# Kernel tuning notes

Hardware: AMD Instinct MI355X
Metric: run time of the kernel (lower is better)

## Reference

```python
import jax, jax.numpy as jnp
import numpy as np

B, S, D = 8, 1024, 768
H, DH = 8, 96          # number_of_heads, head_outdim = D // H
DFF = 4 * D            # mlp hidden
EPS = 1e-5


def _p(key, shape, scale=0.02):
    return (jax.random.normal(key, shape, dtype=jnp.float32) * scale)


def setup_inputs() -> dict:
    key = jax.random.key(0)
    ks = jax.random.split(key, 16)
    return {
        "h": jax.random.normal(ks[0], (B, S, D), dtype=jnp.float32),
        "x": jax.random.normal(ks[1], (B, S, D), dtype=jnp.float32),
        # SLN 1: scalar gamma/beta + LayerNorm affine
        "g1": jnp.ones((), jnp.float32), "be1": jnp.zeros((), jnp.float32),
        "ln1_w": jnp.ones((D,), jnp.float32), "ln1_b": jnp.zeros((D,), jnp.float32),
        # SLN 2
        "g2": jnp.ones((), jnp.float32), "be2": jnp.zeros((), jnp.float32),
        "ln2_w": jnp.ones((D,), jnp.float32), "ln2_b": jnp.zeros((D,), jnp.float32),
        # MSA projections (stored as [in, out] for x @ W)
        "Wq": _p(ks[2], (D, H * DH)), "bq": jnp.zeros((H * DH,), jnp.float32),
        "Wk": _p(ks[3], (D, H * DH)), "bk": jnp.zeros((H * DH,), jnp.float32),
        "Wv": _p(ks[4], (D, H * DH)), "bv": jnp.zeros((H * DH,), jnp.float32),
        "Wo": _p(ks[5], (H * DH, D)), "bo": jnp.zeros((D,), jnp.float32),
        # MLP: D -> 4D -> D, relu
        "W1": _p(ks[6], (D, DFF)), "b1": jnp.zeros((DFF,), jnp.float32),
        "W2": _p(ks[7], (DFF, D)), "b2": jnp.zeros((D,), jnp.float32),
    }


def _sln(h, x, gamma, beta, w, b):
    # SLN(h, x) = gamma * x * LayerNorm(h) + beta * x
    mu = jnp.mean(h, axis=-1, keepdims=True)
    var = jnp.var(h, axis=-1, keepdims=True)
    ln = (h - mu) * jax.lax.rsqrt(var + EPS) * w + b
    return gamma * x * ln + beta * x


def _l2_msa(h, Wq, bq, Wk, bk, Wv, bv, Wo, bo):
    # L2-distance multi-head self-attention (lp=2)
    def heads(W, bias):
        y = h @ W + bias                      # [B,S,H*DH]
        return y.reshape(B, S, H, DH).transpose(0, 2, 1, 3)  # [B,H,S,DH]
    q, k, v = heads(Wq, bq), heads(Wk, bk), heads(Wv, bv)
    # pairwise L2 distances via the quadratic expansion (avoids [B,H,S,S,DH])
    q2 = jnp.sum(q * q, axis=-1)              # [B,H,S]
    k2 = jnp.sum(k * k, axis=-1)              # [B,H,S]
    qk = jnp.einsum("bhsd,bhtd->bhst", q, k)  # [B,H,S,S]
    d2 = jnp.maximum(q2[..., :, None] + k2[..., None, :] - 2.0 * qk, 0.0)
    dist = jnp.sqrt(d2)                       # cdist(q, k, p=2)
    attn = jax.nn.softmax(-dist / np.sqrt(DH), axis=-1)
    out = jnp.einsum("bhst,bhtd->bhsd", attn, v)  # [B,H,S,DH]
    out = out.transpose(0, 2, 1, 3).reshape(B, S, H * DH)
    return out @ Wo + bo


def reference(h, x, g1, be1, ln1_w, ln1_b, g2, be2, ln2_w, ln2_b,
              Wq, bq, Wk, bk, Wv, bv, Wo, bo, W1, b1, W2, b2):
    h1 = _sln(h, x, g1, be1, ln1_w, ln1_b)
    htmp = _l2_msa(h1, Wq, bq, Wk, bk, Wv, bv, Wo, bo) + h   # dropout_rate=0 -> identity
    h2 = _sln(htmp, x, g2, be2, ln2_w, ln2_b)
    hf = jax.nn.relu(h2 @ W1 + b1) @ W2 + b2 + htmp
    return (x, hf)
```

## Files before the change

kernel.cpp:

```cpp
#include <hip/hip_runtime.h>
#include <math.h>

#define B_ 8
#define S_ 1024
#define D_ 768
#define H_ 8
#define DH_ 96
#define DFF_ 3072
#define NTOK (B_*S_)
#define QKVW 2304
#define EPS_ 1e-5f

typedef __attribute__((ext_vector_type(4))) float f4;
typedef __attribute__((ext_vector_type(4))) int i4;
typedef __attribute__((ext_vector_type(8))) __bf16 bf16x8;
typedef __attribute__((ext_vector_type(4))) unsigned short us4;
typedef __attribute__((ext_vector_type(8))) unsigned short us8;

static __device__ __forceinline__ unsigned short f2bf(float f) {
    unsigned int u = __builtin_bit_cast(unsigned int, f);
    u += 0x7fffu + ((u >> 16) & 1u);
    return (unsigned short)(u >> 16);
}
static __device__ __forceinline__ float bf2f(unsigned short u) {
    unsigned int x = ((unsigned int)u) << 16;
    return __builtin_bit_cast(float, x);
}

#define GLOBAL_LOAD_LDS16(g, l) \
    __builtin_amdgcn_global_load_lds((const __attribute__((address_space(1))) unsigned int*)(g), \
                                     (__attribute__((address_space(3))) unsigned int*)(l), 16, 0, 0)

__global__ __launch_bounds__(192) void sln_kernel(
    const float* __restrict__ h, const float* __restrict__ x,
    const float* __restrict__ gamma, const float* __restrict__ beta,
    const float* __restrict__ w, const float* __restrict__ bvec,
    unsigned short* __restrict__ out_bf, float* __restrict__ xcopy)
{
    int row = blockIdx.x;
    int t = threadIdx.x;
    const float4* h4 = (const float4*)(h + (size_t)row * D_);
    const float4* x4 = (const float4*)(x + (size_t)row * D_);
    float4 hv = h4[t];
    float s  = hv.x + hv.y + hv.z + hv.w;
    float ss = hv.x*hv.x + hv.y*hv.y + hv.z*hv.z + hv.w*hv.w;
    #pragma unroll
    for (int off = 32; off > 0; off >>= 1) {
        s  += __shfl_down(s, off);
        ss += __shfl_down(ss, off);
    }
    __shared__ float red[2][3];
    int wid = t >> 6;
    if ((t & 63) == 0) { red[0][wid] = s; red[1][wid] = ss; }
    __syncthreads();
    float sum   = red[0][0] + red[0][1] + red[0][2];
    float sumsq = red[1][0] + red[1][1] + red[1][2];
    float mu  = sum * (1.0f / D_);
    float var = sumsq * (1.0f / D_) - mu * mu;
    float rstd = rsqrtf(var + EPS_);
    float g = gamma[0], be = beta[0];
    float4 wv = ((const float4*)w)[t];
    float4 bv = ((const float4*)bvec)[t];
    float4 xv = x4[t];
    us4 o;
    o.x = f2bf(xv.x * (g * ((hv.x - mu) * rstd * wv.x + bv.x) + be));
    o.y = f2bf(xv.y * (g * ((hv.y - mu) * rstd * wv.y + bv.y) + be));
    o.z = f2bf(xv.z * (g * ((hv.z - mu) * rstd * wv.z + bv.z) + be));
    o.w = f2bf(xv.w * (g * ((hv.w - mu) * rstd * wv.w + bv.w) + be));
    *(us4*)(out_bf + (size_t)row * D_ + t * 4) = o;
    if (xcopy) ((float4*)(xcopy + (size_t)row * D_))[t] = xv;
}

__global__ __launch_bounds__(256) void transpose_bf16_kernel(
    const float* __restrict__ in, unsigned short* __restrict__ out, int K, int N)
{
    __shared__ float tile[32][33];
    int n0 = blockIdx.x * 32, k0 = blockIdx.y * 32;
    int tx = threadIdx.x, ty = threadIdx.y;
    #pragma unroll
    for (int r = 0; r < 4; r++)
        tile[ty + r * 8][tx] = in[(size_t)(k0 + ty + r * 8) * N + n0 + tx];
    __syncthreads();
    #pragma unroll
    for (int r = 0; r < 4; r++)
        out[(size_t)(n0 + ty + r * 8) * K + k0 + tx] = f2bf(tile[tx][ty + r * 8]);
}

__global__ void concat_bias_kernel(const float* __restrict__ bq, const float* __restrict__ bk,
                                   const float* __restrict__ bv, float* __restrict__ outb)
{
    int i = blockIdx.x * 256 + threadIdx.x;
    if (i >= QKVW) return;
    float v = (i < 768) ? bq[i] : (i < 1536) ? bk[i - 768] : bv[i - 1536];
    outb[i] = v;
}

template<int OUT_BF16, int RELU>
__global__ __launch_bounds__(256) void gemm_mfma_kernel(
    const unsigned short* __restrict__ A, const unsigned short* __restrict__ Bt,
    const float* __restrict__ bias, const float* __restrict__ resid,
    void* __restrict__ Cout, int M, int N, int K)
{
    __shared__ unsigned short Asm[128 * 32];
    __shared__ unsigned short Bsm[128 * 32];

    int t = threadIdx.x;
    int lane = t & 63, wv = t >> 6;
    int wm = wv & 1, wn = wv >> 1;
    int l16 = lane & 15, quad = lane >> 4;

    int bm = blockIdx.x * 128;
    int bn = blockIdx.y * 128;

    const unsigned short* Abase = A  + (size_t)bm * K;
    const unsigned short* Bbase = Bt + (size_t)bn * K;

    int fl0 = t, fl1 = 256 + t;
    int r0s = fl0 >> 2, kc0 = (fl0 & 3) << 3;
    int r1s = fl1 >> 2, kc1 = (fl1 & 3) << 3;

    f4 acc[4][4] = {};

    for (int k0 = 0; k0 < K; k0 += 32) {
        __syncthreads();
        GLOBAL_LOAD_LDS16(Abase + (size_t)r0s * K + k0 + kc0, &Asm[fl0 * 8]);
        GLOBAL_LOAD_LDS16(Abase + (size_t)r1s * K + k0 + kc1, &Asm[fl1 * 8]);
        GLOBAL_LOAD_LDS16(Bbase + (size_t)r0s * K + k0 + kc0, &Bsm[fl0 * 8]);
        GLOBAL_LOAD_LDS16(Bbase + (size_t)r1s * K + k0 + kc1, &Bsm[fl1 * 8]);
        __syncthreads();

        bf16x8 xf[4], wf[4];
        #pragma unroll
        for (int i = 0; i < 4; i++) {
            int m = wm * 64 + i * 16 + l16;
            xf[i] = __builtin_bit_cast(bf16x8, *(const i4*)&Asm[m * 32 + quad * 8]);
        }
        #pragma unroll
        for (int j = 0; j < 4; j++) {
            int n = wn * 64 + j * 16 + l16;
            wf[j] = __builtin_bit_cast(bf16x8, *(const i4*)&Bsm[n * 32 + quad * 8]);
        }
        #pragma unroll
        for (int j = 0; j < 4; j++)
            #pragma unroll
            for (int i = 0; i < 4; i++)
                acc[j][i] = __builtin_amdgcn_mfma_f32_16x16x32_bf16(wf[j], xf[i], acc[j][i], 0, 0, 0);
    }

    #pragma unroll
    for (int i = 0; i < 4; i++) {
        int rowg = bm + wm * 64 + i * 16 + l16;
        #pragma unroll
        for (int j = 0; j < 4; j++) {
            int colg0 = bn + wn * 64 + j * 16 + quad * 4;
            f4 v = acc[j][i];
            f4 b4 = *(const f4*)&bias[colg0];
            v += b4;
            if (RELU) {
                #pragma unroll
                for (int r = 0; r < 4; r++) v[r] = fmaxf(v[r], 0.f);
            }
            if (resid) {
                f4 r4 = *(const f4*)&resid[(size_t)rowg * N + colg0];
                v += r4;
            }
            if (OUT_BF16) {
                us4 o;
                o.x = f2bf(v[0]); o.y = f2bf(v[1]); o.z = f2bf(v[2]); o.w = f2bf(v[3]);
                *(us4*)((unsigned short*)Cout + (size_t)rowg * N + colg0) = o;
            } else {
                *(f4*)((float*)Cout + (size_t)rowg * N + colg0) = v;
            }
        }
    }
}

template<int OUT_BF16, int RELU>
__global__ __launch_bounds__(256) void gemm_mfma_n64_kernel(
    const unsigned short* __restrict__ A, const unsigned short* __restrict__ Bt,
    const float* __restrict__ bias, const float* __restrict__ resid,
    void* __restrict__ Cout, int M, int N, int K)
{
    __shared__ unsigned short Asm[128 * 32];
    __shared__ unsigned short Bsm[64 * 32];

    int t = threadIdx.x;
    int lane = t & 63, wv = t >> 6;
    int wm = wv & 1, wn = wv >> 1;
    int l16 = lane & 15, quad = lane >> 4;

    int bm = blockIdx.x * 128;
    int bn = blockIdx.y * 64;

    const unsigned short* Abase = A  + (size_t)bm * K;
    const unsigned short* Bbase = Bt + (size_t)bn * K;

    int fl0 = t, fl1 = 256 + t;
    int r0s = fl0 >> 2, kc0 = (fl0 & 3) << 3;
    int r1s = fl1 >> 2, kc1 = (fl1 & 3) << 3;

    f4 acc[2][4] = {};

    for (int k0 = 0; k0 < K; k0 += 32) {
        __syncthreads();
        GLOBAL_LOAD_LDS16(Abase + (size_t)r0s * K + k0 + kc0, &Asm[fl0 * 8]);
        GLOBAL_LOAD_LDS16(Abase + (size_t)r1s * K + k0 + kc1, &Asm[fl1 * 8]);
        GLOBAL_LOAD_LDS16(Bbase + (size_t)r0s * K + k0 + kc0, &Bsm[fl0 * 8]);
        __syncthreads();

        bf16x8 xf[4], wf[2];
        #pragma unroll
        for (int i = 0; i < 4; i++) {
            int m = wm * 64 + i * 16 + l16;
            xf[i] = __builtin_bit_cast(bf16x8, *(const i4*)&Asm[m * 32 + quad * 8]);
        }
        #pragma unroll
        for (int j = 0; j < 2; j++) {
            int n = wn * 32 + j * 16 + l16;
            wf[j] = __builtin_bit_cast(bf16x8, *(const i4*)&Bsm[n * 32 + quad * 8]);
        }
        #pragma unroll
        for (int j = 0; j < 2; j++)
            #pragma unroll
            for (int i = 0; i < 4; i++)
                acc[j][i] = __builtin_amdgcn_mfma_f32_16x16x32_bf16(wf[j], xf[i], acc[j][i], 0, 0, 0);
    }

    #pragma unroll
    for (int i = 0; i < 4; i++) {
        int rowg = bm + wm * 64 + i * 16 + l16;
        #pragma unroll
        for (int j = 0; j < 2; j++) {
            int colg0 = bn + wn * 32 + j * 16 + quad * 4;
            f4 v = acc[j][i];
            f4 b4 = *(const f4*)&bias[colg0];
            v += b4;
            if (RELU) {
                #pragma unroll
                for (int r = 0; r < 4; r++) v[r] = fmaxf(v[r], 0.f);
            }
            if (resid) {
                f4 r4 = *(const f4*)&resid[(size_t)rowg * N + colg0];
                v += r4;
            }
            if (OUT_BF16) {
                us4 o;
                o.x = f2bf(v[0]); o.y = f2bf(v[1]); o.z = f2bf(v[2]); o.w = f2bf(v[3]);
                *(us4*)((unsigned short*)Cout + (size_t)rowg * N + colg0) = o;
            } else {
                *(f4*)((float*)Cout + (size_t)rowg * N + colg0) = v;
            }
        }
    }
}

__global__ __launch_bounds__(256) void norms_kernel(
    const unsigned short* __restrict__ qkv, float* __restrict__ q2g, float* __restrict__ k2g)
{
    int row = blockIdx.x;
    int t = threadIdx.x;
    int hh = t >> 5, l32 = t & 31;
    const unsigned short* base = qkv + (size_t)row * QKVW + hh * DH_ + l32 * 3;
    float qs = 0.f, ks = 0.f;
    #pragma unroll
    for (int e = 0; e < 3; e++) {
        float qv = bf2f(base[e]);
        float kv = bf2f(base[768 + e]);
        qs += qv * qv; ks += kv * kv;
    }
    #pragma unroll
    for (int off = 16; off > 0; off >>= 1) {
        qs += __shfl_xor(qs, off, 32);
        ks += __shfl_xor(ks, off, 32);
    }
    if (l32 == 0) {
        int b = row >> 10, s = row & 1023;
        int idx = (b * H_ + hh) * S_ + s;
        q2g[idx] = qs; k2g[idx] = ks;
    }
}

__global__ __launch_bounds__(256) void vtrans_kernel(
    const unsigned short* __restrict__ qkv, unsigned short* __restrict__ vt)
{
    __shared__ unsigned short Vl[64][100];
    int blk = blockIdx.x;
    int bh = blk >> 4, kt = blk & 15;
    int b = bh >> 3, hh = bh & 7;
    int t = threadIdx.x;
    int key = t >> 2, qc = t & 3;
    const unsigned short* src = qkv + ((size_t)(b * S_ + kt * 64 + key)) * QKVW + 1536 + hh * DH_;
    #pragma unroll
    for (int i = 0; i < 3; i++) {
        int chunk = qc + i * 4;
        us8 v = *(const us8*)(src + chunk * 8);
        #pragma unroll
        for (int e = 0; e < 8; e++) Vl[key][chunk * 8 + e] = v[e];
    }
    __syncthreads();
    unsigned short* dst = vt + (size_t)blk * 7168;
    #pragma unroll
    for (int r = 0; r < 3; r++) {
        int c = r * 256 + t;
        int vd = c >> 3, kc = c & 7;
        us8 o;
        #pragma unroll
        for (int j = 0; j < 8; j++) o[j] = Vl[kc * 8 + j][vd];
        *(us8*)(dst + vd * 72 + kc * 8) = o;
    }
}

__global__ __launch_bounds__(256, 4) void attn_mfma_kernel(
    const unsigned short* __restrict__ qkv,
    const unsigned short* __restrict__ vt,
    const float* __restrict__ q2g, const float* __restrict__ k2g,
    unsigned short* __restrict__ outb)
{
    __shared__ unsigned short Klds[64 * 96];
    __shared__ unsigned short Vlds[7168];
    __shared__ unsigned short Plds[4][16 * 72];

    int t = threadIdx.x;
    int lane = t & 63, w = t >> 6;
    int l16 = lane & 15, quad = lane >> 4;

    int bh = blockIdx.x >> 4;
    int qt = blockIdx.x & 15;
    int b = bh >> 3, hh = bh & 7;

    int qrow0 = qt * 64 + w * 16;

    const unsigned short* qb = qkv + ((size_t)(b * S_ + qrow0)) * QKVW + hh * DH_;
    bf16x8 qf[3];
    #pragma unroll
    for (int d = 0; d < 3; d++)
        qf[d] = __builtin_bit_cast(bf16x8,
            *(const i4*)(qb + (size_t)l16 * QKVW + d * 32 + quad * 8));

    float q2n = q2g[bh * S_ + qrow0 + l16];

    float mrun = -INFINITY;
    float lrun = 0.f;
    f4 Oacc[6] = {};

    const float cexp = 0.14724445f;

    const unsigned short* kgb = qkv + ((size_t)(b * S_)) * QKVW + 768 + hh * DH_;
    const unsigned short* vgb0 = vt + (size_t)(bh * 16) * 7168;

    for (int it = 0; it < 16; it++) {
        __syncthreads();
        #pragma unroll
        for (int r = 0; r < 3; r++) {
            int c = r * 256 + t;
            int key = c / 12, dc = c % 12;
            GLOBAL_LOAD_LDS16(kgb + ((size_t)(it * 64 + key)) * QKVW + dc * 8, &Klds[c * 8]);
        }
        const unsigned short* vgb = vgb0 + (size_t)it * 7168;
        #pragma unroll
        for (int r = 0; r < 3; r++)
            GLOBAL_LOAD_LDS16(vgb + (r * 256 + t) * 8, &Vlds[(r * 256 + t) * 8]);
        if (t < 128)
            GLOBAL_LOAD_LDS16(vgb + (768 + t) * 8, &Vlds[(768 + t) * 8]);
        __syncthreads();

        f4 sf[4];
        #pragma unroll
        for (int kt2 = 0; kt2 < 4; kt2++) {
            bf16x8 kf0 = __builtin_bit_cast(bf16x8, *(const i4*)&Klds[(kt2 * 16 + l16) * 96 + quad * 8]);
            bf16x8 kf1 = __builtin_bit_cast(bf16x8, *(const i4*)&Klds[(kt2 * 16 + l16) * 96 + 32 + quad * 8]);
            bf16x8 kf2 = __builtin_bit_cast(bf16x8, *(const i4*)&Klds[(kt2 * 16 + l16) * 96 + 64 + quad * 8]);
            f4 a = {};
            a = __builtin_amdgcn_mfma_f32_16x16x32_bf16(kf0, qf[0], a, 0, 0, 0);
            a = __builtin_amdgcn_mfma_f32_16x16x32_bf16(kf1, qf[1], a, 0, 0, 0);
            a = __builtin_amdgcn_mfma_f32_16x16x32_bf16(kf2, qf[2], a, 0, 0, 0);
            sf[kt2] = a;
        }
        #pragma unroll
        for (int kt2 = 0; kt2 < 4; kt2++) {
            float4 k2f = *(const float4*)(k2g + bh * S_ + it * 64 + kt2 * 16 + quad * 4);
            float k2a[4] = {k2f.x, k2f.y, k2f.z, k2f.w};
            f4 s = sf[kt2];
            #pragma unroll
            for (int r2 = 0; r2 < 4; r2++) {
                float d2 = fmaxf(q2n + k2a[r2] - 2.f * s[r2], 0.f);
                s[r2] = -__builtin_amdgcn_sqrtf(d2) * cexp;
            }
            sf[kt2] = s;
        }
        f4 m4 = sf[0];
        #pragma unroll
        for (int kt2 = 1; kt2 < 4; kt2++)
            #pragma unroll
            for (int r2 = 0; r2 < 4; r2++)
                m4[r2] = fmaxf(m4[r2], sf[kt2][r2]);
        float mx = fmaxf(fmaxf(m4[0], m4[1]), fmaxf(m4[2], m4[3]));
        mx = fmaxf(mx, __shfl_xor(mx, 16, 64));
        mx = fmaxf(mx, __shfl_xor(mx, 32, 64));
        float mnew = fmaxf(mrun, mx);
        float alph = exp2f(mrun - mnew);
        mrun = mnew;
        float ssum = 0.f;
        #pragma unroll
        for (int kt2 = 0; kt2 < 4; kt2++) {
            f4 s = sf[kt2];
            #pragma unroll
            for (int r2 = 0; r2 < 4; r2++) { s[r2] = exp2f(s[r2] - mnew); ssum += s[r2]; }
            sf[kt2] = s;
        }
        ssum += __shfl_xor(ssum, 16, 64);
        ssum += __shfl_xor(ssum, 32, 64);
        lrun = lrun * alph + ssum;
        #pragma unroll
        for (int kt2 = 0; kt2 < 4; kt2++) {
            f4 s = sf[kt2];
            uint2 pk;
            pk.x = (unsigned)f2bf(s[0]) | ((unsigned)f2bf(s[1]) << 16);
            pk.y = (unsigned)f2bf(s[2]) | ((unsigned)f2bf(s[3]) << 16);
            *(uint2*)&Plds[w][l16 * 72 + kt2 * 16 + quad * 4] = pk;
        }
        f4 av;
        #pragma unroll
        for (int r2 = 0; r2 < 4; r2++)
            av[r2] = __shfl(alph, quad * 4 + r2, 64);
        #pragma unroll
        for (int vtl = 0; vtl < 6; vtl++)
            #pragma unroll
            for (int r2 = 0; r2 < 4; r2++)
                Oacc[vtl][r2] *= av[r2];
        bf16x8 pa0 = __builtin_bit_cast(bf16x8, *(const i4*)&Plds[w][l16 * 72 + quad * 8]);
        bf16x8 pa1 = __builtin_bit_cast(bf16x8, *(const i4*)&Plds[w][l16 * 72 + 32 + quad * 8]);
        #pragma unroll
        for (int vtl = 0; vtl < 6; vtl++) {
            bf16x8 vf0 = __builtin_bit_cast(bf16x8, *(const i4*)&Vlds[(vtl * 16 + l16) * 72 + quad * 8]);
            bf16x8 vf1 = __builtin_bit_cast(bf16x8, *(const i4*)&Vlds[(vtl * 16 + l16) * 72 + 32 + quad * 8]);
            Oacc[vtl] = __builtin_amdgcn_mfma_f32_16x16x32_bf16(pa0, vf0, Oacc[vtl], 0, 0, 0);
            Oacc[vtl] = __builtin_amdgcn_mfma_f32_16x16x32_bf16(pa1, vf1, Oacc[vtl], 0, 0, 0);
        }
    }
    float inv_l = 1.f / lrun;
    f4 iv;
    #pragma unroll
    for (int r2 = 0; r2 < 4; r2++)
        iv[r2] = __shfl(inv_l, quad * 4 + r2, 64);
    #pragma unroll
    for (int vtl = 0; vtl < 6; vtl++)
        #pragma unroll
        for (int r2 = 0; r2 < 4; r2++) {
            int row = b * S_ + qrow0 + quad * 4 + r2;
            outb[(size_t)row * D_ + hh * DH_ + vtl * 16 + l16] = f2bf(Oacc[vtl][r2] * iv[r2]);
        }
}

extern "C" void kernel_launch(void* const* d_in, const int* in_sizes, int n_in,
                              void* d_out, int out_size, void* d_ws, size_t ws_size,
                              hipStream_t stream)
{
    const float* h    = (const float*)d_in[0];
    const float* x    = (const float*)d_in[1];
    const float* g1   = (const float*)d_in[2];
    const float* be1  = (const float*)d_in[3];
    const float* ln1w = (const float*)d_in[4];
    const float* ln1b = (const float*)d_in[5];
    const float* g2   = (const float*)d_in[6];
    const float* be2  = (const float*)d_in[7];
    const float* ln2w = (const float*)d_in[8];
    const float* ln2b = (const float*)d_in[9];
    const float* Wq   = (const float*)d_in[10];
    const float* bq   = (const float*)d_in[11];
    const float* Wk   = (const float*)d_in[12];
    const float* bk   = (const float*)d_in[13];
    const float* Wv   = (const float*)d_in[14];
    const float* bv   = (const float*)d_in[15];
    const float* Wo   = (const float*)d_in[16];
    const float* bo   = (const float*)d_in[17];
    const float* W1   = (const float*)d_in[18];
    const float* b1   = (const float*)d_in[19];
    const float* W2   = (const float*)d_in[20];
    const float* b2   = (const float*)d_in[21];

    float* out = (float*)d_out;
    char* wsb = (char*)d_ws;
    const size_t ND = (size_t)NTOK * D_;

    size_t off = 0;
    unsigned short* W1t = (unsigned short*)(wsb + off); off += 4718592;
    unsigned short* W2t = (unsigned short*)(wsb + off); off += 4718592;
    float* bqkv = (float*)(wsb + off);                  off += 16384;
    float* htmp = (float*)(wsb + off);                  off += ND * 4;
    float* q2g  = (float*)(wsb + off);                  off += (size_t)B_ * H_ * S_ * 4;
    float* k2g  = (float*)(wsb + off);                  off += (size_t)B_ * H_ * S_ * 4;
    unsigned short* h2b = (unsigned short*)(wsb + off); off += ND * 2;
    size_t pool0 = off;
    unsigned short* Wqkvt = (unsigned short*)(wsb + off); off += 3538944;
    unsigned short* Wot   = (unsigned short*)(wsb + off); off += 1179648;
    unsigned short* h1b   = (unsigned short*)(wsb + off); off += ND * 2;
    unsigned short* vtg   = (unsigned short*)(wsb + off); off += (size_t)1024 * 14336;
    unsigned short* qkvb  = (unsigned short*)(wsb + off); off += (size_t)NTOK * QKVW * 2;
    unsigned short* attnb   = h1b;
    unsigned short* hiddenb = (unsigned short*)(wsb + pool0);

    dim3 tb(32, 8);
    transpose_bf16_kernel<<<dim3(768/32, 768/32), tb, 0, stream>>>(Wq, Wqkvt,              768, 768);
    transpose_bf16_kernel<<<dim3(768/32, 768/32), tb, 0, stream>>>(Wk, Wqkvt + 768*768,    768, 768);
    transpose_bf16_kernel<<<dim3(768/32, 768/32), tb, 0, stream>>>(Wv, Wqkvt + 2*768*768,  768, 768);
    transpose_bf16_kernel<<<dim3(768/32, 768/32), tb, 0, stream>>>(Wo, Wot, 768, 768);
    transpose_bf16_kernel<<<dim3(3072/32, 768/32), tb, 0, stream>>>(W1, W1t, 768, 3072);
    transpose_bf16_kernel<<<dim3(768/32, 3072/32), tb, 0, stream>>>(W2, W2t, 3072, 768);
    concat_bias_kernel<<<9, 256, 0, stream>>>(bq, bk, bv, bqkv);

    sln_kernel<<<NTOK, 192, 0, stream>>>(h, x, g1, be1, ln1w, ln1b, h1b, out);

    gemm_mfma_kernel<1, 0><<<dim3(NTOK/128, QKVW/128), 256, 0, stream>>>(
        h1b, Wqkvt, bqkv, nullptr, qkvb, NTOK, QKVW, D_);

    norms_kernel<<<NTOK, 256, 0, stream>>>(qkvb, q2g, k2g);
    vtrans_kernel<<<1024, 256, 0, stream>>>(qkvb, vtg);

    attn_mfma_kernel<<<1024, 256, 0, stream>>>(qkvb, vtg, q2g, k2g, attnb);

    gemm_mfma_n64_kernel<0, 0><<<dim3(NTOK/128, D_/64), 256, 0, stream>>>(
        attnb, Wot, bo, h, htmp, NTOK, D_, D_);

    sln_kernel<<<NTOK, 192, 0, stream>>>(htmp, x, g2, be2, ln2w, ln2b, h2b, nullptr);

    gemm_mfma_kernel<1, 1><<<dim3(NTOK/128, DFF_/128), 256, 0, stream>>>(
        h2b, W1t, b1, nullptr, hiddenb, NTOK, DFF_, D_);
    gemm_mfma_n64_kernel<0, 0><<<dim3(NTOK/128, D_/64), 256, 0, stream>>>(
        hiddenb, W2t, b2, htmp, out + ND, NTOK, D_, DFF_);

    (void)in_sizes; (void)n_in; (void)out_size; (void)ws_size;
}
```

Before: 468.7 us.

## Drop online-softmax max tracking in L2 attention and merge weight-prep launches

Because the scores are negated scaled distances, every score is at most zero, so exp2 of a score cannot overflow. The attention kernel therefore drops the running max, the rescale factor and the per-tile accumulator rescaling. It fuses the distance, exp and P packing into the QK loop and reduces the row sum once at the end. Separately, the six weight transpose launches and the bias concat are merged into one kernel that indexes by block, cutting launch overhead. The risk is underflow: rows whose distances are all large could sum to near zero, although with cexp near 0.147 this is unlikely for realistic distances.

Result: faster. 453.5 us (-3.2%).

```diff
diff --git a/kernel.cpp b/kernel.cpp
--- a/kernel.cpp
+++ b/kernel.cpp
@@ -71,12 +71,34 @@
     if (xcopy) ((float4*)(xcopy + (size_t)row * D_))[t] = xv;
 }
 
-__global__ __launch_bounds__(256) void transpose_bf16_kernel(
-    const float* __restrict__ in, unsigned short* __restrict__ out, int K, int N)
-{
+__global__ __launch_bounds__(256) void prep_all_kernel(
+    const float* __restrict__ Wq, const float* __restrict__ Wk,
+    const float* __restrict__ Wv, const float* __restrict__ Wo,
+    const float* __restrict__ W1, const float* __restrict__ W2,
+    const float* __restrict__ bq, const float* __restrict__ bk, const float* __restrict__ bv,
+    unsigned short* __restrict__ Wqkvt, unsigned short* __restrict__ Wot,
+    unsigned short* __restrict__ W1t, unsigned short* __restrict__ W2t,
+    float* __restrict__ bqkv)
+{
+    int id = blockIdx.x;
+    int tx = threadIdx.x, ty = threadIdx.y;
+    if (id >= 6912) {
+        int i = (id - 6912) * 256 + ty * 32 + tx;
+        if (i < QKVW) {
+            float v = (i < 768) ? bq[i] : (i < 1536) ? bk[i - 768] : bv[i - 1536];
+            bqkv[i] = v;
+        }
+        return;
+    }
+    const float* in; unsigned short* out; int K, N, nbx, rel;
+    if (id < 1728)      { int m = id / 576; rel = id % 576;
+                          in = (m == 0) ? Wq : (m == 1) ? Wk : Wv;
+                          out = Wqkvt + (size_t)m * 768 * 768; K = 768; N = 768; nbx = 24; }
+    else if (id < 2304) { rel = id - 1728; in = Wo; out = Wot;  K = 768;  N = 768;  nbx = 24; }
+    else if (id < 4608) { rel = id - 2304; in = W1; out = W1t;  K = 768;  N = 3072; nbx = 96; }
+    else                { rel = id - 4608; in = W2; out = W2t;  K = 3072; N = 768;  nbx = 24; }
+    int n0 = (rel % nbx) * 32, k0 = (rel / nbx) * 32;
     __shared__ float tile[32][33];
-    int n0 = blockIdx.x * 32, k0 = blockIdx.y * 32;
-    int tx = threadIdx.x, ty = threadIdx.y;
     #pragma unroll
     for (int r = 0; r < 4; r++)
         tile[ty + r * 8][tx] = in[(size_t)(k0 + ty + r * 8) * N + n0 + tx];
@@ -84,15 +106,6 @@
     #pragma unroll
     for (int r = 0; r < 4; r++)
         out[(size_t)(n0 + ty + r * 8) * K + k0 + tx] = f2bf(tile[tx][ty + r * 8]);
-}
-
-__global__ void concat_bias_kernel(const float* __restrict__ bq, const float* __restrict__ bk,
-                                   const float* __restrict__ bv, float* __restrict__ outb)
-{
-    int i = blockIdx.x * 256 + threadIdx.x;
-    if (i >= QKVW) return;
-    float v = (i < 768) ? bq[i] : (i < 1536) ? bk[i - 768] : bv[i - 1536];
-    outb[i] = v;
 }
 
 template<int OUT_BF16, int RELU>
@@ -339,8 +352,7 @@
 
     float q2n = q2g[bh * S_ + qrow0 + l16];
 
-    float mrun = -INFINITY;
-    float lrun = 0.f;
+    float lsum = 0.f;
     f4 Oacc[6] = {};
 
     const float cexp = 0.14724445f;
@@ -364,7 +376,6 @@
             GLOBAL_LOAD_LDS16(vgb + (768 + t) * 8, &Vlds[(768 + t) * 8]);
         __syncthreads();
 
-        f4 sf[4];
         #pragma unroll
         for (int kt2 = 0; kt2 < 4; kt2++) {
             bf16x8 kf0 = __builtin_bit_cast(bf16x8, *(const i4*)&Klds[(kt2 * 16 + l16) * 96 + quad * 8]);
@@ -374,60 +385,20 @@
             a = __builtin_amdgcn_mfma_f32_16x16x32_bf16(kf0, qf[0], a, 0, 0, 0);
             a = __builtin_amdgcn_mfma_f32_16x16x32_bf16(kf1, qf[1], a, 0, 0, 0);
             a = __builtin_amdgcn_mfma_f32_16x16x32_bf16(kf2, qf[2], a, 0, 0, 0);
-            sf[kt2] = a;
-        }
-        #pragma unroll
-        for (int kt2 = 0; kt2 < 4; kt2++) {
             float4 k2f = *(const float4*)(k2g + bh * S_ + it * 64 + kt2 * 16 + quad * 4);
-            float k2a[4] = {k2f.x, k2f.y, k2f.z, k2f.w};
-            f4 s = sf[kt2];
+            float pk2[4] = {k2f.x + q2n, k2f.y + q2n, k2f.z + q2n, k2f.w + q2n};
             #pragma unroll
             for (int r2 = 0; r2 < 4; r2++) {
-                float d2 = fmaxf(q2n + k2a[r2] - 2.f * s[r2], 0.f);
-                s[r2] = -__builtin_amdgcn_sqrtf(d2) * cexp;
-            }
-            sf[kt2] = s;
-        }
-        f4 m4 = sf[0];
-        #pragma unroll
-        for (int kt2 = 1; kt2 < 4; kt2++)
-            #pragma unroll
-            for (int r2 = 0; r2 < 4; r2++)
-                m4[r2] = fmaxf(m4[r2], sf[kt2][r2]);
-        float mx = fmaxf(fmaxf(m4[0], m4[1]), fmaxf(m4[2], m4[3]));
-        mx = fmaxf(mx, __shfl_xor(mx, 16, 64));
-        mx = fmaxf(mx, __shfl_xor(mx, 32, 64));
-        float mnew = fmaxf(mrun, mx);
-        float alph = exp2f(mrun - mnew);
-        mrun = mnew;
-        float ssum = 0.f;
-        #pragma unroll
-        for (int kt2 = 0; kt2 < 4; kt2++) {
-            f4 s = sf[kt2];
-            #pragma unroll
-            for (int r2 = 0; r2 < 4; r2++) { s[r2] = exp2f(s[r2] - mnew); ssum += s[r2]; }
-            sf[kt2] = s;
-        }
-        ssum += __shfl_xor(ssum, 16, 64);
-        ssum += __shfl_xor(ssum, 32, 64);
-        lrun = lrun * alph + ssum;
-        #pragma unroll
-        for (int kt2 = 0; kt2 < 4; kt2++) {
-            f4 s = sf[kt2];
-            uint2 pk;
-            pk.x = (unsigned)f2bf(s[0]) | ((unsigned)f2bf(s[1]) << 16);
-            pk.y = (unsigned)f2bf(s[2]) | ((unsigned)f2bf(s[3]) << 16);
-            *(uint2*)&Plds[w][l16 * 72 + kt2 * 16 + quad * 4] = pk;
-        }
-        f4 av;
-        #pragma unroll
-        for (int r2 = 0; r2 < 4; r2++)
-            av[r2] = __shfl(alph, quad * 4 + r2, 64);
-        #pragma unroll
-        for (int vtl = 0; vtl < 6; vtl++)
-            #pragma unroll
-            for (int r2 = 0; r2 < 4; r2++)
-                Oacc[vtl][r2] *= av[r2];
+                float d2 = fmaxf(pk2[r2] - 2.f * a[r2], 0.f);
+                float p = exp2f(-__builtin_amdgcn_sqrtf(d2) * cexp);
+                lsum += p;
+                a[r2] = p;
+            }
+            uint2 pkd;
+            pkd.x = (unsigned)f2bf(a[0]) | ((unsigned)f2bf(a[1]) << 16);
+            pkd.y = (unsigned)f2bf(a[2]) | ((unsigned)f2bf(a[3]) << 16);
+            *(uint2*)&Plds[w][l16 * 72 + kt2 * 16 + quad * 4] = pkd;
+        }
         bf16x8 pa0 = __builtin_bit_cast(bf16x8, *(const i4*)&Plds[w][l16 * 72 + quad * 8]);
         bf16x8 pa1 = __builtin_bit_cast(bf16x8, *(const i4*)&Plds[w][l16 * 72 + 32 + quad * 8]);
         #pragma unroll
@@ -438,7 +409,9 @@
             Oacc[vtl] = __builtin_amdgcn_mfma_f32_16x16x32_bf16(pa1, vf1, Oacc[vtl], 0, 0, 0);
         }
     }
-    float inv_l = 1.f / lrun;
+    lsum += __shfl_xor(lsum, 16, 64);
+    lsum += __shfl_xor(lsum, 32, 64);
+    float inv_l = 1.f / lsum;
     f4 iv;
     #pragma unroll
     for (int r2 = 0; r2 < 4; r2++)
@@ -500,14 +473,8 @@
     unsigned short* attnb   = h1b;
     unsigned short* hiddenb = (unsigned short*)(wsb + pool0);
 
-    dim3 tb(32, 8);
-    transpose_bf16_kernel<<<dim3(768/32, 768/32), tb, 0, stream>>>(Wq, Wqkvt,              768, 768);
-    transpose_bf16_kernel<<<dim3(768/32, 768/32), tb, 0, stream>>>(Wk, Wqkvt + 768*768,    768, 768);
-    transpose_bf16_kernel<<<dim3(768/32, 768/32), tb, 0, stream>>>(Wv, Wqkvt + 2*768*768,  768, 768);
-    transpose_bf16_kernel<<<dim3(768/32, 768/32), tb, 0, stream>>>(Wo, Wot, 768, 768);
-    transpose_bf16_kernel<<<dim3(3072/32, 768/32), tb, 0, stream>>>(W1, W1t, 768, 3072);
-    transpose_bf16_kernel<<<dim3(768/32, 3072/32), tb, 0, stream>>>(W2, W2t, 3072, 768);
-    concat_bias_kernel<<<9, 256, 0, stream>>>(bq, bk, bv, bqkv);
+    prep_all_kernel<<<6921, dim3(32, 8), 0, stream>>>(
+        Wq, Wk, Wv, Wo, W1, W2, bq, bk, bv, Wqkvt, Wot, W1t, W2t, bqkv);
 
     sln_kernel<<<NTOK, 192, 0, stream>>>(h, x, g1, be1, ln1w, ln1b, h1b, out);
 
```
